# Kernel tuning notes

Hardware: AMD Instinct MI355X
Metric: run time of the kernel (lower is better)

Reference implementation:

```python
import jax, jax.numpy as jnp
import numpy as np

EMBEDDING_DIM = 256
SCALE_STEP = 2
NUM_SCALES = EMBEDDING_DIM // 4  # 64


def setup_inputs() -> dict:
    key = jax.random.key(0)
    B = 500000
    # lat/lon in degrees (roughly earth-like ranges via scaled normal)
    lat_lon_deg = jax.random.normal(key, (B, 2), dtype=jnp.float32) * 45.0
    return {"lat_lon_deg": lat_lon_deg}


def reference(lat_lon_deg):
    B = lat_lon_deg.shape[0]
    rad = jnp.deg2rad(lat_lon_deg)                       # [B, 2]
    scales = (SCALE_STEP ** jnp.arange(NUM_SCALES)).astype(rad.dtype)  # [S]
    lat = rad[:, 0:1] * scales                           # [B, S]
    lon = rad[:, 1:2] * scales                           # [B, S]
    # per scale layout: [sin(lat), cos(lat), sin(lon), cos(lon)]
    feats = jnp.stack(
        [jnp.sin(lat), jnp.cos(lat), jnp.sin(lon), jnp.cos(lon)], axis=-1
    )                                                    # [B, S, 4]
    features = feats.reshape(B, 1, NUM_SCALES * 4)       # [B, 1, 256]
    mask = jnp.zeros((B, 1), dtype=bool)
    positions = jnp.zeros((B, 1, 1, 2), dtype=features.dtype)
    return features, mask, positions
```

## Files before the change

### kernel.cpp

```cpp
#include <hip/hip_runtime.h>


typedef float f32x4 __attribute__((ext_vector_type(4)));

#define PTS_PER_BLOCK 64
#define ZERO_BLOCKS   128

__global__ __launch_bounds__(256) void posfeat_kernel(const float* __restrict__ ll,
                                                      f32x4* __restrict__ out,
                                                      int B, long long n4) {
    const double QHI = 0x1.45F306DC9C883p-3;
    const float DEG2RAD = 0.017453292519943295f;
    const long long featUnits = (long long)B * 64;

    if (blockIdx.x < ZERO_BLOCKS) {
        const f32x4 ZERO4 = {0.f, 0.f, 0.f, 0.f};
        const long long stride = (long long)ZERO_BLOCKS * 256;
        for (long long z = featUnits + (long long)blockIdx.x * 256 + threadIdx.x;
             z < n4; z += stride)
            __builtin_nontemporal_store(ZERO4, &out[z]);
        return;
    }

    __shared__ double yll[PTS_PER_BLOCK][2];
    const int fb = blockIdx.x - ZERO_BLOCKS;
    const int p0 = fb * PTS_PER_BLOCK;
    const int t = threadIdx.x;

    if (t < PTS_PER_BLOCK) {
        int b = p0 + t;
        float2 p = (b < B) ? reinterpret_cast<const float2*>(ll)[b]
                           : make_float2(0.f, 0.f);
        float rlat = p.x * DEG2RAD;
        float rlon = p.y * DEG2RAD;
        yll[t][0] = (double)rlat * QHI;
        yll[t][1] = (double)rlon * QHI;
    }
    __syncthreads();

    const long long ubase = (long long)p0 * 64;
    const int s = t & 63;
    #pragma unroll
    for (int i = 0; i < (PTS_PER_BLOCK * 64) / 256; ++i) {
        int idx = i * 256 + t;
        long long u = ubase + idx;
        if (u >= featUnits) break;
        int pl = idx >> 6;
        double ya = yll[pl][0], yb = yll[pl][1];
        double va = ldexp(ya, s), vb = ldexp(yb, s);
        if (s == 31) { va = -va; vb = -vb; }
        double fa = va - floor(va), fb2 = vb - floor(vb);
        float ra = (float)fa, rb = (float)fb2;
        f32x4 o;
        o.x = __builtin_amdgcn_sinf(ra);
        o.y = __builtin_amdgcn_cosf(ra);
        o.z = __builtin_amdgcn_sinf(rb);
        o.w = __builtin_amdgcn_cosf(rb);
        if (s >= 32) { o = (f32x4){0.f, 1.f, 0.f, 1.f}; }
        __builtin_nontemporal_store(o, &out[u]);
    }
}

__global__ void tail_zero_kernel(float* __restrict__ z, int n) {
    int t = threadIdx.x;
    if (t < n) z[t] = 0.f;
}

extern "C" void kernel_launch(void* const* d_in, const int* in_sizes, int n_in,
                              void* d_out, int out_size, void* d_ws, size_t ws_size,
                              hipStream_t stream) {
    const float* ll = (const float*)d_in[0];
    float* out = (float*)d_out;
    int B = in_sizes[0] / 2;

    long long n4 = (long long)out_size >> 2;
    int featBlocks = (B + PTS_PER_BLOCK - 1) / PTS_PER_BLOCK;
    posfeat_kernel<<<featBlocks + ZERO_BLOCKS, 256, 0, stream>>>(ll, (f32x4*)out, B, n4);

    int tail = out_size & 3;
    if (tail) {
        tail_zero_kernel<<<1, 64, 0, stream>>>(out + ((long long)out_size - tail), tail);
    }
}
```

Measured before the change: 108.0 us.

## Replace per-element double range reduction with 64-bit fixed-point shifts

The scaled angle (in turns) is precomputed once per point as a 64-bit fixed-point fraction in shared memory. Each scale's reduced argument is then taken with integer shifts instead of double-precision ldexp and floor per element. Threads now cover only the 32 non-constant scales and store the constant {0,1,0,1} for the upper 32 scales directly, with 128 points per block. This removes the FP64 work from the inner loop, at the cost of a different rounding path to float and two strided stores per iteration.

```diff
diff --git a/kernel.cpp b/kernel.cpp
--- a/kernel.cpp
+++ b/kernel.cpp
@@ -3,8 +3,8 @@
 
 typedef float f32x4 __attribute__((ext_vector_type(4)));
 
-#define PTS_PER_BLOCK 64
-#define ZERO_BLOCKS   128
+#define PTS 128
+#define ZERO_BLOCKS 128
 
 __global__ __launch_bounds__(256) void posfeat_kernel(const float* __restrict__ ll,
                                                       f32x4* __restrict__ out,
@@ -22,42 +22,53 @@
         return;
     }
 
-    __shared__ double yll[PTS_PER_BLOCK][2];
-    const int fb = blockIdx.x - ZERO_BLOCKS;
-    const int p0 = fb * PTS_PER_BLOCK;
+    __shared__ uint4 yfix[PTS];
+    const int p0 = (blockIdx.x - ZERO_BLOCKS) * PTS;
     const int t = threadIdx.x;
 
-    if (t < PTS_PER_BLOCK) {
+    if (t < PTS) {
         int b = p0 + t;
         float2 p = (b < B) ? reinterpret_cast<const float2*>(ll)[b]
                            : make_float2(0.f, 0.f);
         float rlat = p.x * DEG2RAD;
         float rlon = p.y * DEG2RAD;
-        yll[t][0] = (double)rlat * QHI;
-        yll[t][1] = (double)rlon * QHI;
+        double ya = (double)rlat * QHI; ya -= floor(ya);
+        double yb = (double)rlon * QHI; yb -= floor(yb);
+        double sa = ya * 4294967296.0;
+        unsigned ha = (unsigned)sa;
+        unsigned la = (unsigned)((sa - (double)ha) * 4294967296.0);
+        double sb = yb * 4294967296.0;
+        unsigned hb = (unsigned)sb;
+        unsigned lb = (unsigned)((sb - (double)hb) * 4294967296.0);
+        yfix[t] = make_uint4(ha, la, hb, lb);
     }
     __syncthreads();
 
-    const long long ubase = (long long)p0 * 64;
-    const int s = t & 63;
+    const f32x4 CONST4 = {0.f, 1.f, 0.f, 1.f};
+    const int s = t & 31;
+    const int po = t >> 5;
+    const unsigned sh = (32 - s) & 31;
+
     #pragma unroll
-    for (int i = 0; i < (PTS_PER_BLOCK * 64) / 256; ++i) {
-        int idx = i * 256 + t;
-        long long u = ubase + idx;
-        if (u >= featUnits) break;
-        int pl = idx >> 6;
-        double ya = yll[pl][0], yb = yll[pl][1];
-        double va = ldexp(ya, s), vb = ldexp(yb, s);
-        if (s == 31) { va = -va; vb = -vb; }
-        double fa = va - floor(va), fb2 = vb - floor(vb);
-        float ra = (float)fa, rb = (float)fb2;
+    for (int i = 0; i < PTS / 8; ++i) {
+        int pl = i * 8 + po;
+        int b = p0 + pl;
+        uint4 Y = yfix[pl];
+        unsigned ra_u = (Y.x << s) | ((s == 0) ? 0u : (Y.y >> sh));
+        unsigned rb_u = (Y.z << s) | ((s == 0) ? 0u : (Y.w >> sh));
+        float ra = (float)ra_u * 0x1.0p-32f;
+        float rb = (float)rb_u * 0x1.0p-32f;
+        if (s == 31) { ra = -ra; rb = -rb; }
         f32x4 o;
         o.x = __builtin_amdgcn_sinf(ra);
         o.y = __builtin_amdgcn_cosf(ra);
         o.z = __builtin_amdgcn_sinf(rb);
         o.w = __builtin_amdgcn_cosf(rb);
-        if (s >= 32) { o = (f32x4){0.f, 1.f, 0.f, 1.f}; }
-        __builtin_nontemporal_store(o, &out[u]);
+        if (b < B) {
+            long long base = ((long long)b << 6) + s;
+            __builtin_nontemporal_store(o, &out[base]);
+            __builtin_nontemporal_store(CONST4, &out[base + 32]);
+        }
     }
 }
 
@@ -74,7 +85,7 @@
     int B = in_sizes[0] / 2;
 
     long long n4 = (long long)out_size >> 2;
-    int featBlocks = (B + PTS_PER_BLOCK - 1) / PTS_PER_BLOCK;
+    int featBlocks = (B + PTS - 1) / PTS;
     posfeat_kernel<<<featBlocks + ZERO_BLOCKS, 256, 0, stream>>>(ll, (f32x4*)out, B, n4);
 
     int tail = out_size & 3;
```

Result: faster. 100.9 us (-6.6%).
